# Kernel tuning notes

Hardware: AMD Instinct MI355X
Metric: run time of the kernel (lower is better)

## Reference

```python
import jax, jax.numpy as jnp
import numpy as np
from jax import lax

B, T, D, H, O = 4096, 128, 128, 150, 10

def setup_inputs() -> dict:
    key = jax.random.key(0)
    k1, k2, k3 = jax.random.split(key, 3)
    X = jax.random.normal(k1, (B, T, D), dtype=jnp.float32)
    # BasicRNNCell kernel: acts on concat([x, h]) -> [D+H, H]
    W_cell = jax.random.normal(k2, (D + H, H), dtype=jnp.float32) * (1.0 / np.sqrt(D + H))
    b_cell = jnp.zeros((H,), dtype=jnp.float32)
    W_out = jax.random.normal(k3, (H, O), dtype=jnp.float32) * (1.0 / np.sqrt(H))
    b_out = jnp.zeros((O,), dtype=jnp.float32)
    return {"X": X, "W_cell": W_cell, "b_cell": b_cell, "W_out": W_out, "b_out": b_out}

def reference(X, W_cell, b_cell, W_out, b_out):
    # dynamic_rnn with BasicRNNCell: h_t = tanh([x_t, h_{t-1}] @ W + b)
    batch = X.shape[0]
    hid = W_cell.shape[1]
    xs = jnp.swapaxes(X, 0, 1)  # [T, B, D]
    h0 = jnp.zeros((batch, hid), dtype=X.dtype)

    def step(h, x_t):
        h_new = jnp.tanh(jnp.concatenate([x_t, h], axis=-1) @ W_cell + b_cell)
        return h_new, None

    h_final, _ = lax.scan(step, h0, xs)
    # dense classifier on final state (tf code applies dense to `states`)
    logits = h_final @ W_out + b_out  # [B, O]
    return logits
```

## Files before the change

### kernel.cpp

```cpp
#include <hip/hip_runtime.h>
#include <hip/hip_bf16.h>


typedef __bf16 bf16x8 __attribute__((ext_vector_type(8)));
typedef float  f32x4  __attribute__((ext_vector_type(4)));
typedef float  f32x8  __attribute__((ext_vector_type(8)));

#define B_  4096
#define T_  128
#define D_  128
#define H_  150
#define O_  10

#define KX 4
#define KH 5
#define HPAD 168

__global__ __launch_bounds__(320) void rnn_fused(
    const float* __restrict__ X,
    const float* __restrict__ Wc,
    const float* __restrict__ bc,
    const float* __restrict__ Wo,
    const float* __restrict__ bo,
    float* __restrict__ out)
{
    __shared__ __attribute__((aligned(16))) __bf16 sh_h[2][16][HPAD];

    const int tid  = threadIdx.x;
    const int wid  = tid >> 6;
    const int lane = tid & 63;
    const int q    = lane >> 4;
    const int l16  = lane & 15;
    const int row0 = blockIdx.x * 16;

    {
        __bf16* p = &sh_h[0][0][0];
        for (int i = tid; i < 2 * 16 * HPAD; i += 320) p[i] = (__bf16)0.f;
    }

    bf16x8 wx[2][KX];
    bf16x8 wh[2][KH];
    float  bias[2];
    int    jc[2];
#pragma unroll
    for (int nt = 0; nt < 2; ++nt) {
        const int  j   = wid * 32 + nt * 16 + l16;
        const bool jv  = (j < H_);
        const int  jcl = jv ? j : 0;
        jc[nt]   = j;
        bias[nt] = jv ? bc[jcl] : 0.f;
#pragma unroll
        for (int kt = 0; kt < KX; ++kt) {
            bf16x8 f;
#pragma unroll
            for (int i = 0; i < 8; ++i) {
                const int k = kt * 32 + q * 8 + i;
                float v = Wc[k * H_ + jcl];
                v = fminf(fmaxf(v, -64.f), 64.f);
                f[i] = jv ? (__bf16)v : (__bf16)0.f;
            }
            wx[nt][kt] = f;
        }
#pragma unroll
        for (int kt = 0; kt < KH; ++kt) {
            bf16x8 f;
#pragma unroll
            for (int i = 0; i < 8; ++i) {
                const int  kh  = kt * 32 + q * 8 + i;
                const bool kv  = jv && (kh < H_);
                const int  khc = (kh < H_) ? kh : 0;
                float v = Wc[(D_ + khc) * H_ + jcl];
                v = fminf(fmaxf(v, -64.f), 64.f);
                f[i] = kv ? (__bf16)v : (__bf16)0.f;
            }
            wh[nt][kt] = f;
        }
    }

    __syncthreads();

    const float* xrow = X + (size_t)(row0 + l16) * (T_ * D_) + q * 8;

    f32x8 xb0[KX], xb1[KX];
#pragma unroll
    for (int kt = 0; kt < KX; ++kt) xb0[kt] = *(const f32x8*)(xrow + 0 * D_ + kt * 32);
#pragma unroll
    for (int kt = 0; kt < KX; ++kt) xb1[kt] = *(const f32x8*)(xrow + 1 * D_ + kt * 32);

    auto step = [&](int t, f32x8 (&xb)[KX]) {
        bf16x8 a[KX];
#pragma unroll
        for (int kt = 0; kt < KX; ++kt) {
#pragma unroll
            for (int i = 0; i < 8; ++i) {
                float c = xb[kt][i];
                c = fminf(fmaxf(c, -64.f), 64.f);
                a[kt][i] = (__bf16)c;
            }
        }
        f32x4 acc0 = {bias[0], bias[0], bias[0], bias[0]};
        f32x4 acc1 = {bias[1], bias[1], bias[1], bias[1]};
#pragma unroll
        for (int kt = 0; kt < KX; ++kt) {
            acc0 = __builtin_amdgcn_mfma_f32_16x16x32_bf16(a[kt], wx[0][kt], acc0, 0, 0, 0);
            acc1 = __builtin_amdgcn_mfma_f32_16x16x32_bf16(a[kt], wx[1][kt], acc1, 0, 0, 0);
        }
        {
            int tt = t + 2; tt = (tt > T_ - 1) ? (T_ - 1) : tt;
#pragma unroll
            for (int kt = 0; kt < KX; ++kt)
                xb[kt] = *(const f32x8*)(xrow + (size_t)tt * D_ + kt * 32);
        }
        const __bf16 (*hb)[HPAD] = sh_h[t & 1];
#pragma unroll
        for (int kt = 0; kt < KH; ++kt) {
            bf16x8 ah = *(const bf16x8*)(&hb[l16][kt * 32 + q * 8]);
            acc0 = __builtin_amdgcn_mfma_f32_16x16x32_bf16(ah, wh[0][kt], acc0, 0, 0, 0);
            acc1 = __builtin_amdgcn_mfma_f32_16x16x32_bf16(ah, wh[1][kt], acc1, 0, 0, 0);
        }
        __bf16 (*ho)[HPAD] = sh_h[(t + 1) & 1];
#pragma unroll
        for (int r = 0; r < 4; ++r) {
            const int rr = q * 4 + r;
            {
                float z = acc0[r];
                float e = __expf(z + z);
                float hv = 1.f - 2.f * __builtin_amdgcn_rcpf(e + 1.f);
                ho[rr][jc[0]] = (__bf16)hv;
            }
            {
                float z = acc1[r];
                float e = __expf(z + z);
                float hv = 1.f - 2.f * __builtin_amdgcn_rcpf(e + 1.f);
                ho[rr][jc[1]] = (__bf16)hv;
            }
        }
        __syncthreads();
    };

    for (int t = 0; t < T_; t += 2) {
        step(t,     xb0);
        step(t + 1, xb1);
    }

    if (tid < 16 * O_) {
        const int row = tid / O_;
        const int o   = tid - row * O_;
        float accv = bo[o];
        const __bf16* hf = &sh_h[0][row][0];
        for (int k = 0; k < H_; ++k)
            accv += (float)hf[k] * Wo[k * O_ + o];
        out[(size_t)(row0 + row) * O_ + o] = accv;
    }
}

extern "C" void kernel_launch(void* const* d_in, const int* in_sizes, int n_in,
                              void* d_out, int out_size, void* d_ws, size_t ws_size,
                              hipStream_t stream) {
    (void)in_sizes; (void)n_in; (void)out_size; (void)d_ws; (void)ws_size;
    const float* X  = (const float*)d_in[0];
    const float* Wc = (const float*)d_in[1];
    const float* bc = (const float*)d_in[2];
    const float* Wo = (const float*)d_in[3];
    const float* bo = (const float*)d_in[4];
    rnn_fused<<<dim3(B_ / 16), dim3(320), 0, stream>>>(X, Wc, bc, Wo, bo, (float*)d_out);
}
```

Baseline: 470.9 us.

## Split x/h MFMA accumulators, hoist LDS loads, pack h stores, lighter barrier

Loads the previous hidden state from LDS at the start of each step so the reads overlap with the X conversion and prefetch. The input and recurrent MFMA chains now use separate accumulators, which shortens the dependency chain at the cost of an extra add. Each lane's columns are remapped so it owns two adjacent columns, letting it write one packed 32-bit LDS store per row instead of two scalar bf16 stores. The per-step clamps on X are dropped, tanh uses exp2 directly, and __syncthreads is replaced by an inline-asm waitcnt plus barrier. The manual barrier relies on the compiler not reordering memory around it, and omitting the clamp could matter for extreme input values.

Result: faster. 455.7 us (-3.2%).

```diff
diff --git a/kernel.cpp b/kernel.cpp
--- a/kernel.cpp
+++ b/kernel.cpp
@@ -5,6 +5,7 @@
 typedef __bf16 bf16x8 __attribute__((ext_vector_type(8)));
 typedef float  f32x4  __attribute__((ext_vector_type(4)));
 typedef float  f32x8  __attribute__((ext_vector_type(8)));
+typedef unsigned short u16;
 
 #define B_  4096
 #define T_  128
@@ -41,13 +42,12 @@
     bf16x8 wx[2][KX];
     bf16x8 wh[2][KH];
     float  bias[2];
-    int    jc[2];
+    const int colw = wid * 32 + 2 * l16;
 #pragma unroll
     for (int nt = 0; nt < 2; ++nt) {
-        const int  j   = wid * 32 + nt * 16 + l16;
+        const int  j   = colw + nt;
         const bool jv  = (j < H_);
         const int  jcl = jv ? j : 0;
-        jc[nt]   = j;
         bias[nt] = jv ? bc[jcl] : 0.f;
 #pragma unroll
         for (int kt = 0; kt < KX; ++kt) {
@@ -88,60 +88,65 @@
     for (int kt = 0; kt < KX; ++kt) xb1[kt] = *(const f32x8*)(xrow + 1 * D_ + kt * 32);
 
     auto step = [&](int t, f32x8 (&xb)[KX]) {
+        const __bf16 (*hb)[HPAD] = sh_h[t & 1];
+        bf16x8 ah[KH];
+#pragma unroll
+        for (int kt = 0; kt < KH; ++kt)
+            ah[kt] = *(const bf16x8*)(&hb[l16][kt * 32 + q * 8]);
+
         bf16x8 a[KX];
 #pragma unroll
         for (int kt = 0; kt < KX; ++kt) {
 #pragma unroll
-            for (int i = 0; i < 8; ++i) {
-                float c = xb[kt][i];
-                c = fminf(fmaxf(c, -64.f), 64.f);
-                a[kt][i] = (__bf16)c;
-            }
+            for (int i = 0; i < 8; ++i)
+                a[kt][i] = (__bf16)xb[kt][i];
         }
-        f32x4 acc0 = {bias[0], bias[0], bias[0], bias[0]};
-        f32x4 acc1 = {bias[1], bias[1], bias[1], bias[1]};
-#pragma unroll
-        for (int kt = 0; kt < KX; ++kt) {
-            acc0 = __builtin_amdgcn_mfma_f32_16x16x32_bf16(a[kt], wx[0][kt], acc0, 0, 0, 0);
-            acc1 = __builtin_amdgcn_mfma_f32_16x16x32_bf16(a[kt], wx[1][kt], acc1, 0, 0, 0);
-        }
+
         {
             int tt = t + 2; tt = (tt > T_ - 1) ? (T_ - 1) : tt;
 #pragma unroll
             for (int kt = 0; kt < KX; ++kt)
                 xb[kt] = *(const f32x8*)(xrow + (size_t)tt * D_ + kt * 32);
         }
-        const __bf16 (*hb)[HPAD] = sh_h[t & 1];
+
+        f32x4 ax0 = {bias[0], bias[0], bias[0], bias[0]};
+        f32x4 ax1 = {bias[1], bias[1], bias[1], bias[1]};
+        f32x4 ah0 = {0.f, 0.f, 0.f, 0.f};
+        f32x4 ah1 = {0.f, 0.f, 0.f, 0.f};
+#pragma unroll
+        for (int kt = 0; kt < KX; ++kt) {
+            ax0 = __builtin_amdgcn_mfma_f32_16x16x32_bf16(a[kt], wx[0][kt], ax0, 0, 0, 0);
+            ax1 = __builtin_amdgcn_mfma_f32_16x16x32_bf16(a[kt], wx[1][kt], ax1, 0, 0, 0);
+        }
 #pragma unroll
         for (int kt = 0; kt < KH; ++kt) {
-            bf16x8 ah = *(const bf16x8*)(&hb[l16][kt * 32 + q * 8]);
-            acc0 = __builtin_amdgcn_mfma_f32_16x16x32_bf16(ah, wh[0][kt], acc0, 0, 0, 0);
-            acc1 = __builtin_amdgcn_mfma_f32_16x16x32_bf16(ah, wh[1][kt], acc1, 0, 0, 0);
+            ah0 = __builtin_amdgcn_mfma_f32_16x16x32_bf16(ah[kt], wh[0][kt], ah0, 0, 0, 0);
+            ah1 = __builtin_amdgcn_mfma_f32_16x16x32_bf16(ah[kt], wh[1][kt], ah1, 0, 0, 0);
         }
+
         __bf16 (*ho)[HPAD] = sh_h[(t + 1) & 1];
 #pragma unroll
         for (int r = 0; r < 4; ++r) {
-            const int rr = q * 4 + r;
-            {
-                float z = acc0[r];
-                float e = __expf(z + z);
-                float hv = 1.f - 2.f * __builtin_amdgcn_rcpf(e + 1.f);
-                ho[rr][jc[0]] = (__bf16)hv;
-            }
-            {
-                float z = acc1[r];
-                float e = __expf(z + z);
-                float hv = 1.f - 2.f * __builtin_amdgcn_rcpf(e + 1.f);
-                ho[rr][jc[1]] = (__bf16)hv;
-            }
+            const float z0 = ax0[r] + ah0[r];
+            const float z1 = ax1[r] + ah1[r];
+            const float e0 = __builtin_amdgcn_exp2f(z0 * 2.8853900817779268f);
+            const float e1 = __builtin_amdgcn_exp2f(z1 * 2.8853900817779268f);
+            const float h0 = 1.f - 2.f * __builtin_amdgcn_rcpf(e0 + 1.f);
+            const float h1 = 1.f - 2.f * __builtin_amdgcn_rcpf(e1 + 1.f);
+            const unsigned p = (unsigned)__builtin_bit_cast(u16, (__bf16)h0)
+                             | ((unsigned)__builtin_bit_cast(u16, (__bf16)h1) << 16);
+            *(unsigned*)(&ho[q * 4 + r][colw]) = p;
         }
-        __syncthreads();
+
+        asm volatile("s_waitcnt lgkmcnt(0)\n\ts_barrier" ::: "memory");
     };
 
     for (int t = 0; t < T_; t += 2) {
         step(t,     xb0);
         step(t + 1, xb1);
     }
+
+    __syncthreads();
 
     if (tid < 16 * O_) {
         const int row = tid / O_;
```
